# Kernel optimization log

Hardware: AMD Instinct MI355X
Metric: run time of the kernel (lower is better)

The kernel has to match this reference:

```python
import jax, jax.numpy as jnp
import numpy as np

N_NODES = 100000


def _sage_conv(x, src, dst, Wl, Wr, b):
    # mean aggregation of source features onto destination nodes (PyG SAGEConv default)
    msgs = x[src]                                             # [E, d] irregular gather
    agg = jax.ops.segment_sum(msgs, dst, num_segments=N_NODES)
    cnt = jax.ops.segment_sum(jnp.ones((src.shape[0], 1), x.dtype), dst,
                              num_segments=N_NODES)
    agg = agg / jnp.maximum(cnt, 1.0)                         # mean; isolated nodes -> 0
    return agg @ Wl.T + x @ Wr.T + b                          # W_l * agg + W_r * x + b


def setup_inputs() -> dict:
    key = jax.random.key(0)
    ks = jax.random.split(key, 7)
    d_in, d_hid, d_out = 64, 64, 40
    n_edges = 1200000
    x = jax.random.normal(ks[0], (N_NODES, d_in), dtype=jnp.float32)
    edge_index = jax.random.randint(ks[1], (2, n_edges), 0, N_NODES, dtype=jnp.int64)
    s1 = 1.0 / np.sqrt(d_in)
    s2 = 1.0 / np.sqrt(d_hid)
    return {
        "x": x,
        "edge_index": edge_index,
        "W1l": jax.random.normal(ks[2], (d_hid, d_in), dtype=jnp.float32) * s1,
        "W1r": jax.random.normal(ks[3], (d_hid, d_in), dtype=jnp.float32) * s1,
        "b1": jnp.zeros((d_hid,), dtype=jnp.float32),
        "W2l": jax.random.normal(ks[4], (d_out, d_hid), dtype=jnp.float32) * s2,
        "W2r": jax.random.normal(ks[5], (d_out, d_hid), dtype=jnp.float32) * s2,
        "b2": jnp.zeros((d_out,), dtype=jnp.float32),
    }


def reference(x, edge_index, W1l, W1r, b1, W2l, W2r, b2):
    src, dst = edge_index[0], edge_index[1]
    h = _sage_conv(x, src, dst, W1l, W1r, b1)
    h = jax.nn.relu(h)
    # F.dropout(p=0.5) in eval mode is identity (deterministic reference)
    out = _sage_conv(h, src, dst, W2l, W2r, b2)
    return out
```

## Files before the change

kernel.cpp:

```cpp
#include <hip/hip_runtime.h>
#include <hip/hip_bf16.h>

__device__ __forceinline__ float bf2f(unsigned short u) {
    return __uint_as_float(((unsigned int)u) << 16);
}
__device__ __forceinline__ unsigned short f2bf(float f) {
    unsigned int u = __float_as_uint(f);
    return (unsigned short)((u + 0x7FFFu + ((u >> 16) & 1u)) >> 16);
}

__device__ __forceinline__ bool is_i64(const int* __restrict__ e) {
    int z = 0;
#pragma unroll
    for (int i = 0; i < 16; ++i) z |= e[2 * i + 1];
    return z == 0;
}

__global__ void hist_rank_kernel(const int* __restrict__ eidx, int n_edges,
                                 int* __restrict__ deg, int* __restrict__ rank) {
    const int half = (n_edges + 1) / 2;
    const int e = blockIdx.x * blockDim.x + threadIdx.x;
    if (e >= half) return;
    const bool i64 = is_i64(eidx);
    {
        int d = i64 ? eidx[2 * (n_edges + e)] : eidx[n_edges + e];
        rank[e] = atomicAdd(&deg[d], 1);
    }
    const int e2 = e + half;
    if (e2 < n_edges) {
        int d = i64 ? eidx[2 * (n_edges + e2)] : eidx[n_edges + e2];
        rank[e2] = atomicAdd(&deg[d], 1);
    }
}

__global__ void fill_rank_kernel(const int* __restrict__ eidx, int n_edges,
                                 const int* __restrict__ off, const int* __restrict__ rank,
                                 int* __restrict__ csr) {
    const int half = (n_edges + 1) / 2;
    const int e = blockIdx.x * blockDim.x + threadIdx.x;
    if (e >= half) return;
    const bool i64 = is_i64(eidx);
    {
        int s, d;
        if (i64) { s = eidx[2 * e]; d = eidx[2 * (n_edges + e)]; }
        else     { s = eidx[e];     d = eidx[n_edges + e]; }
        __builtin_nontemporal_store(s, &csr[off[d] + rank[e]]);
    }
    const int e2 = e + half;
    if (e2 < n_edges) {
        int s, d;
        if (i64) { s = eidx[2 * e2]; d = eidx[2 * (n_edges + e2)]; }
        else     { s = eidx[e2];     d = eidx[n_edges + e2]; }
        __builtin_nontemporal_store(s, &csr[off[d] + rank[e2]]);
    }
}

__global__ void fill_kernel(const int* __restrict__ eidx, int n_edges,
                            int* __restrict__ cursor, int* __restrict__ csr) {
    int e = blockIdx.x * blockDim.x + threadIdx.x;
    if (e >= n_edges) return;
    const bool i64 = is_i64(eidx);
    int s, d;
    if (i64) { s = eidx[2 * e]; d = eidx[2 * (n_edges + e)]; }
    else     { s = eidx[e];     d = eidx[n_edges + e]; }
    int pos = atomicAdd(&cursor[d], 1);
    csr[pos] = s;
}

#define TILE 1024
__global__ void scan_p1(const int* __restrict__ deg, int* __restrict__ bsum, int n) {
    __shared__ int red[256];
    const int t = threadIdx.x;
    const int base = blockIdx.x * TILE + t * 4;
    int s = 0;
#pragma unroll
    for (int k = 0; k < 4; ++k) { int i = base + k; if (i < n) s += deg[i]; }
    red[t] = s;
    __syncthreads();
    for (int d = 128; d > 0; d >>= 1) {
        if (t < d) red[t] += red[t + d];
        __syncthreads();
    }
    if (t == 0) bsum[blockIdx.x] = red[0];
}

__global__ void scan_p2(int* __restrict__ bsum, int* __restrict__ off, int nb, int n) {
    __shared__ int s[1024];
    const int t = threadIdx.x;
    s[t] = (t < nb) ? bsum[t] : 0;
    __syncthreads();
    for (int d = 1; d < 1024; d <<= 1) {
        int v = (t >= d) ? s[t - d] : 0;
        __syncthreads();
        s[t] += v;
        __syncthreads();
    }
    if (t < nb) bsum[t] = (t == 0) ? 0 : s[t - 1];
    if (t == 0) off[n] = s[nb - 1];
}

__global__ void scan_p3(const int* __restrict__ deg, const int* __restrict__ bsum,
                        int* __restrict__ off, int* __restrict__ cursor, int n) {
    __shared__ int red[256];
    const int t = threadIdx.x;
    const int base = blockIdx.x * TILE + t * 4;
    int v0 = 0, v1 = 0, v2 = 0, v3 = 0;
    if (base + 0 < n) v0 = deg[base + 0];
    if (base + 1 < n) v1 = deg[base + 1];
    if (base + 2 < n) v2 = deg[base + 2];
    if (base + 3 < n) v3 = deg[base + 3];
    const int mysum = v0 + v1 + v2 + v3;
    red[t] = mysum;
    __syncthreads();
    for (int d = 1; d < 256; d <<= 1) {
        int u = (t >= d) ? red[t - d] : 0;
        __syncthreads();
        red[t] += u;
        __syncthreads();
    }
    int run = bsum[blockIdx.x] + red[t] - mysum;
    if (base + 0 < n) { off[base + 0] = run; cursor[base + 0] = run; run += v0; }
    if (base + 1 < n) { off[base + 1] = run; cursor[base + 1] = run; run += v1; }
    if (base + 2 < n) { off[base + 2] = run; cursor[base + 2] = run; run += v2; }
    if (base + 3 < n) { off[base + 3] = run; cursor[base + 3] = run; run += v3; }
}

template <int OUT_DIM, int GST>
__global__ __launch_bounds__(256) void dual_gemm3(
        const float* __restrict__ in,
        const float* __restrict__ Wl, const float* __restrict__ Wr,
        const float* __restrict__ bias,
        unsigned short* __restrict__ gout,
        float* __restrict__ sout,
        int n_nodes) {
    __shared__ unsigned int sWp[64][65];
    __shared__ float sB[OUT_DIM];
    __shared__ float sX[4][8][68];

    for (int idx = threadIdx.x; idx < OUT_DIM * 64; idx += 256) {
        const int r = idx >> 6, c = idx & 63;
        sWp[c][r] = (unsigned int)f2bf(Wl[idx]) | ((unsigned int)f2bf(Wr[idx]) << 16);
    }
    if (threadIdx.x < OUT_DIM) sB[threadIdx.x] = bias[threadIdx.x];
    __syncthreads();

    const int g = threadIdx.x >> 6;
    const int j = threadIdx.x & 63;
    const bool jv = (j < OUT_DIM);
    const int jj = jv ? j : 0;
    const int blockBase = blockIdx.x * 128;

#pragma unroll 1
    for (int it = 0; it < 4; ++it) {
        const int nb = blockBase + it * 32 + g * 8;
        if (nb >= n_nodes) break;
#pragma unroll
        for (int n = 0; n < 8; ++n) {
            const int node = nb + n;
            sX[g][n][j] = (node < n_nodes) ? in[(size_t)node * 64 + j] : 0.0f;
        }
        float al[8], ar[8];
#pragma unroll
        for (int n = 0; n < 8; ++n) { al[n] = 0.0f; ar[n] = 0.0f; }

#pragma unroll 2
        for (int q = 0; q < 16; ++q) {
            const unsigned int w0 = sWp[4 * q + 0][jj];
            const unsigned int w1 = sWp[4 * q + 1][jj];
            const unsigned int w2 = sWp[4 * q + 2][jj];
            const unsigned int w3 = sWp[4 * q + 3][jj];
            const float4 x0 = *(const float4*)&sX[g][0][4 * q];
            const float4 x1 = *(const float4*)&sX[g][1][4 * q];
            const float4 x2 = *(const float4*)&sX[g][2][4 * q];
            const float4 x3 = *(const float4*)&sX[g][3][4 * q];
            const float4 x4 = *(const float4*)&sX[g][4][4 * q];
            const float4 x5 = *(const float4*)&sX[g][5][4 * q];
            const float4 x6 = *(const float4*)&sX[g][6][4 * q];
            const float4 x7 = *(const float4*)&sX[g][7][4 * q];
#define DG_STEP(WP, M)                                                         \
            {                                                                  \
                const float wl_ = __uint_as_float((WP) << 16);                 \
                const float wr_ = __uint_as_float((WP) & 0xFFFF0000u);         \
                al[0] = fmaf(x0.M, wl_, al[0]); ar[0] = fmaf(x0.M, wr_, ar[0]);\
                al[1] = fmaf(x1.M, wl_, al[1]); ar[1] = fmaf(x1.M, wr_, ar[1]);\
                al[2] = fmaf(x2.M, wl_, al[2]); ar[2] = fmaf(x2.M, wr_, ar[2]);\
                al[3] = fmaf(x3.M, wl_, al[3]); ar[3] = fmaf(x3.M, wr_, ar[3]);\
                al[4] = fmaf(x4.M, wl_, al[4]); ar[4] = fmaf(x4.M, wr_, ar[4]);\
                al[5] = fmaf(x5.M, wl_, al[5]); ar[5] = fmaf(x5.M, wr_, ar[5]);\
                al[6] = fmaf(x6.M, wl_, al[6]); ar[6] = fmaf(x6.M, wr_, ar[6]);\
                al[7] = fmaf(x7.M, wl_, al[7]); ar[7] = fmaf(x7.M, wr_, ar[7]);\
            }
            DG_STEP(w0, x)
            DG_STEP(w1, y)
            DG_STEP(w2, z)
            DG_STEP(w3, w)
#undef DG_STEP
        }

        const float bb = jv ? sB[jj] : 0.0f;
#pragma unroll
        for (int n = 0; n < 8; ++n) {
            const int node = nb + n;
            if (node < n_nodes) {
                if (jv) {
                    gout[(size_t)node * GST + j] = f2bf(al[n]);
                    sout[(size_t)node * OUT_DIM + j] = ar[n] + bb;
                } else if (j < GST) {
                    gout[(size_t)node * GST + j] = 0;
                }
            }
        }
    }
}

template <int SRC_STRIDE, int CGROUPS, int OUT_DIM, bool RELU>
__global__ __launch_bounds__(256) void gather_addmul_bf16(
        const unsigned short* __restrict__ gsrc,
        const float* __restrict__ sadd,
        const int* __restrict__ off, const int* __restrict__ csr,
        float* __restrict__ out, int n_nodes) {
    const int l = threadIdx.x & 63;
    const int wave = (int)((blockIdx.x * blockDim.x + threadIdx.x) >> 6);
    const int c = l & 15, r = l >> 4;
    const bool cact = (c < CGROUPS);
    const int n0 = wave * 8;

    for (int n = n0; n < n0 + 8; ++n) {
        if (n >= n_nodes) return;
        const int e0 = off[n], e1 = off[n + 1];
        float4 a0 = {0.f,0.f,0.f,0.f}, a1 = a0, a2 = a0, a3 = a0;
        for (int i = e0; i < e1; i += 16) {
            const int i0 = i + r, i1 = i0 + 4, i2 = i0 + 8, i3 = i0 + 12;
            if (cact && i0 < e1) {
                const int s = csr[i0];
                const ushort4 u = *(const ushort4*)(gsrc + (size_t)s * SRC_STRIDE + 4 * c);
                a0.x += bf2f(u.x); a0.y += bf2f(u.y); a0.z += bf2f(u.z); a0.w += bf2f(u.w);
            }
            if (cact && i1 < e1) {
                const int s = csr[i1];
                const ushort4 u = *(const ushort4*)(gsrc + (size_t)s * SRC_STRIDE + 4 * c);
                a1.x += bf2f(u.x); a1.y += bf2f(u.y); a1.z += bf2f(u.z); a1.w += bf2f(u.w);
            }
            if (cact && i2 < e1) {
                const int s = csr[i2];
                const ushort4 u = *(const ushort4*)(gsrc + (size_t)s * SRC_STRIDE + 4 * c);
                a2.x += bf2f(u.x); a2.y += bf2f(u.y); a2.z += bf2f(u.z); a2.w += bf2f(u.w);
            }
            if (cact && i3 < e1) {
                const int s = csr[i3];
                const ushort4 u = *(const ushort4*)(gsrc + (size_t)s * SRC_STRIDE + 4 * c);
                a3.x += bf2f(u.x); a3.y += bf2f(u.y); a3.z += bf2f(u.z); a3.w += bf2f(u.w);
            }
        }
        float4 a;
        a.x = (a0.x + a1.x) + (a2.x + a3.x);
        a.y = (a0.y + a1.y) + (a2.y + a3.y);
        a.z = (a0.z + a1.z) + (a2.z + a3.z);
        a.w = (a0.w + a1.w) + (a2.w + a3.w);
        a.x += __shfl_xor(a.x, 16); a.y += __shfl_xor(a.y, 16);
        a.z += __shfl_xor(a.z, 16); a.w += __shfl_xor(a.w, 16);
        a.x += __shfl_xor(a.x, 32); a.y += __shfl_xor(a.y, 32);
        a.z += __shfl_xor(a.z, 32); a.w += __shfl_xor(a.w, 32);
        const int deg = e1 - e0;
        const float inv = (deg > 0) ? 1.0f / (float)deg : 0.0f;
        if (4 * l < OUT_DIM) {
            const float4 sv = *(const float4*)(sadd + (size_t)n * OUT_DIM + 4 * l);
            float4 o;
            o.x = fmaf(a.x, inv, sv.x);
            o.y = fmaf(a.y, inv, sv.y);
            o.z = fmaf(a.z, inv, sv.z);
            o.w = fmaf(a.w, inv, sv.w);
            if (RELU) {
                o.x = fmaxf(o.x, 0.f); o.y = fmaxf(o.y, 0.f);
                o.z = fmaxf(o.z, 0.f); o.w = fmaxf(o.w, 0.f);
            }
            *(float4*)(out + (size_t)n * OUT_DIM + 4 * l) = o;
        }
    }
}

#define NPB 32
template <int OUT_DIM, bool RELU>
__global__ __launch_bounds__(512, 8) void fused_layer_f4(
        const float* __restrict__ feat,
        const int* __restrict__ off, const int* __restrict__ csr,
        const float* __restrict__ Wl, const float* __restrict__ Wr,
        const float* __restrict__ bias,
        float* __restrict__ out, int n_nodes) {
    __shared__ float sWl[OUT_DIM][65];
    __shared__ float sWr[OUT_DIM][65];
    __shared__ float sB[OUT_DIM];
    __shared__ float sA[8][64];
    __shared__ float sX[8][64];

    for (int idx = threadIdx.x; idx < OUT_DIM * 64; idx += 512) {
        sWl[idx >> 6][idx & 63] = Wl[idx];
        sWr[idx >> 6][idx & 63] = Wr[idx];
    }
    if (threadIdx.x < OUT_DIM) sB[threadIdx.x] = bias[threadIdx.x];
    __syncthreads();

    const int g = threadIdx.x >> 6;
    const int l = threadIdx.x & 63;
    const int c = l & 15, r = l >> 4;
    const int base = blockIdx.x * NPB;

#pragma unroll 1
    for (int it = 0; it < NPB / 8; ++it) {
        const int node = base + it * 8 + g;
        if (node >= n_nodes) break;
        const int e0 = off[node], e1 = off[node + 1];
        const float selfv = feat[(size_t)node * 64 + l];
        float4 a0 = {0.f,0.f,0.f,0.f}, a1 = a0, a2 = a0, a3 = a0;
        for (int i = e0; i < e1; i += 16) {
            const int i0 = i + r, i1 = i0 + 4, i2 = i0 + 8, i3 = i0 + 12;
            if (i0 < e1) { const int s = csr[i0];
                const float4 v = *(const float4*)(feat + (size_t)s * 64 + 4 * c);
                a0.x += v.x; a0.y += v.y; a0.z += v.z; a0.w += v.w; }
            if (i1 < e1) { const int s = csr[i1];
                const float4 v = *(const float4*)(feat + (size_t)s * 64 + 4 * c);
                a1.x += v.x; a1.y += v.y; a1.z += v.z; a1.w += v.w; }
            if (i2 < e1) { const int s = csr[i2];
                const float4 v = *(const float4*)(feat + (size_t)s * 64 + 4 * c);
                a2.x += v.x; a2.y += v.y; a2.z += v.z; a2.w += v.w; }
            if (i3 < e1) { const int s = csr[i3];
                const float4 v = *(const float4*)(feat + (size_t)s * 64 + 4 * c);
                a3.x += v.x; a3.y += v.y; a3.z += v.z; a3.w += v.w; }
        }
        float4 a;
        a.x = (a0.x + a1.x) + (a2.x + a3.x);
        a.y = (a0.y + a1.y) + (a2.y + a3.y);
        a.z = (a0.z + a1.z) + (a2.z + a3.z);
        a.w = (a0.w + a1.w) + (a2.w + a3.w);
        a.x += __shfl_xor(a.x, 16); a.y += __shfl_xor(a.y, 16);
        a.z += __shfl_xor(a.z, 16); a.w += __shfl_xor(a.w, 16);
        a.x += __shfl_xor(a.x, 32); a.y += __shfl_xor(a.y, 32);
        a.z += __shfl_xor(a.z, 32); a.w += __shfl_xor(a.w, 32);
        const int deg = e1 - e0;
        const float inv = (deg > 0) ? 1.0f / (float)deg : 0.0f;
        if (l < 16) {
            float4 s4;
            s4.x = a.x * inv; s4.y = a.y * inv; s4.z = a.z * inv; s4.w = a.w * inv;
            *(float4*)&sA[g][4 * l] = s4;
        }
        sX[g][l] = selfv;
        if (l < OUT_DIM) {
            float acc = sB[l];
#pragma unroll
            for (int k = 0; k < 64; ++k) {
                acc = fmaf(sA[g][k], sWl[l][k], acc);
                acc = fmaf(sX[g][k], sWr[l][k], acc);
            }
            if (RELU) acc = fmaxf(acc, 0.0f);
            out[(size_t)node * OUT_DIM + l] = acc;
        }
    }
}

template <int OUT_DIM, bool RELU, bool FEAT_BF16, bool OUT_BF16>
__global__ __launch_bounds__(512, 8) void fused_layer(
        const void* __restrict__ feat,
        const int* __restrict__ off, const int* __restrict__ csr,
        const float* __restrict__ Wl, const float* __restrict__ Wr,
        const float* __restrict__ bias,
        void* __restrict__ out, int n_nodes) {
    __shared__ float sWl[OUT_DIM][65];
    __shared__ float sWr[OUT_DIM][65];
    __shared__ float sB[OUT_DIM];
    __shared__ float sA[8][64];
    __shared__ float sX[8][64];

    for (int idx = threadIdx.x; idx < OUT_DIM * 64; idx += 512) {
        sWl[idx >> 6][idx & 63] = Wl[idx];
        sWr[idx >> 6][idx & 63] = Wr[idx];
    }
    if (threadIdx.x < OUT_DIM) sB[threadIdx.x] = bias[threadIdx.x];
    __syncthreads();

    const int g = threadIdx.x >> 6;
    const int j = threadIdx.x & 63;
    const int base = blockIdx.x * NPB;

#pragma unroll 1
    for (int it = 0; it < NPB / 8; ++it) {
        const int node = base + it * 8 + g;
        if (node >= n_nodes) break;
        const int e0 = off[node], e1 = off[node + 1];
        float a0 = 0.f, a1 = 0.f, a2 = 0.f, a3 = 0.f;
        int i = e0;
        while (i < e1) {
            const int cnt = ((e1 - i) < 64) ? (e1 - i) : 64;
            const int eid = (j < cnt) ? csr[i + j] : 0;
            int t = 0;
            for (; t + 3 < cnt; t += 4) {
                const int s0 = __shfl(eid, t);
                const int s1 = __shfl(eid, t + 1);
                const int s2 = __shfl(eid, t + 2);
                const int s3 = __shfl(eid, t + 3);
                if (FEAT_BF16) {
                    a0 += bf2f(((const unsigned short*)feat)[(size_t)s0 * 64 + j]);
                    a1 += bf2f(((const unsigned short*)feat)[(size_t)s1 * 64 + j]);
                    a2 += bf2f(((const unsigned short*)feat)[(size_t)s2 * 64 + j]);
                    a3 += bf2f(((const unsigned short*)feat)[(size_t)s3 * 64 + j]);
                } else {
                    a0 += ((const float*)feat)[(size_t)s0 * 64 + j];
                    a1 += ((const float*)feat)[(size_t)s1 * 64 + j];
                    a2 += ((const float*)feat)[(size_t)s2 * 64 + j];
                    a3 += ((const float*)feat)[(size_t)s3 * 64 + j];
                }
            }
            for (; t < cnt; ++t) {
                const int s0 = __shfl(eid, t);
                a0 += FEAT_BF16 ? bf2f(((const unsigned short*)feat)[(size_t)s0 * 64 + j])
                                : ((const float*)feat)[(size_t)s0 * 64 + j];
            }
            i += cnt;
        }
        const int deg = e1 - e0;
        const float inv = (deg > 0) ? 1.0f / (float)deg : 0.0f;
        sA[g][j] = ((a0 + a1) + (a2 + a3)) * inv;
        sX[g][j] = FEAT_BF16 ? bf2f(((const unsigned short*)feat)[(size_t)node * 64 + j])
                             : ((const float*)feat)[(size_t)node * 64 + j];
        if (j < OUT_DIM) {
            float acc = sB[j];
#pragma unroll
            for (int k = 0; k < 64; ++k) {
                acc = fmaf(sA[g][k], sWl[j][k], acc);
                acc = fmaf(sX[g][k], sWr[j][k], acc);
            }
            if (RELU) acc = fmaxf(acc, 0.0f);
            if (OUT_BF16)
                ((unsigned short*)out)[(size_t)node * OUT_DIM + j] = f2bf(acc);
            else
                ((float*)out)[(size_t)node * OUT_DIM + j] = acc;
        }
    }
}

extern "C" void kernel_launch(void* const* d_in, const int* in_sizes, int n_in,
                              void* d_out, int out_size, void* d_ws, size_t ws_size,
                              hipStream_t stream) {
    const float* x   = (const float*)d_in[0];
    const int*   ei  = (const int*)d_in[1];
    const float* W1l = (const float*)d_in[2];
    const float* W1r = (const float*)d_in[3];
    const float* b1  = (const float*)d_in[4];
    const float* W2l = (const float*)d_in[5];
    const float* W2r = (const float*)d_in[6];
    const float* b2  = (const float*)d_in[7];
    float* out = (float*)d_out;

    const int n_nodes = in_sizes[0] / 64;
    const int n_edges = in_sizes[1] / 2;

    const size_t off_b  = (size_t)(n_nodes + 1) * sizeof(int);
    const size_t cur_b  = (size_t)n_nodes * sizeof(int);
    const size_t csr_b  = (size_t)n_edges * sizeof(int);
    const size_t rank_b = (size_t)n_edges * sizeof(int);
    const size_t bsum_b = 1024 * sizeof(int);
    const size_t g1_b   = (size_t)n_nodes * 64 * sizeof(unsigned short);
    const size_t s1_b   = (size_t)n_nodes * 64 * sizeof(float);
    const size_t g2_b   = (size_t)n_nodes * 48 * sizeof(unsigned short);
    const size_t h_b    = (size_t)n_nodes * 64 * sizeof(float);
    const size_t reg1_b = g1_b + s1_b;

    char* p = (char*)d_ws;
    int* off    = (int*)p;  p += off_b;
    int* cursor = (int*)p;  p += cur_b;
    int* csr    = (int*)p;  p += csr_b;
    int* rank   = (int*)p;  p += rank_b;
    int* bsum   = (int*)p;  p += bsum_b;
    size_t used = ((size_t)(p - (char*)d_ws) + 255) / 256 * 256;
    p = (char*)d_ws + used;

    const bool tierA = ws_size >= used + reg1_b + h_b;
    const bool tierC = ws_size >= used + h_b;

    unsigned short* g1 = (unsigned short*)p;
    float*          s1 = (float*)(p + g1_b);
    float*          h  = (float*)(p + reg1_b);
    unsigned short* g2 = (unsigned short*)p;
    float*          s2 = (float*)(p + g2_b);

    hipMemsetAsync(cursor, 0, cur_b, stream);
    const int half = (n_edges + 1) / 2;
    const int hblocks = (half + 255) / 256;
    hist_rank_kernel<<<hblocks, 256, 0, stream>>>(ei, n_edges, cursor, rank);
    const int nb = (n_nodes + TILE - 1) / TILE;
    scan_p1<<<nb, 256, 0, stream>>>(cursor, bsum, n_nodes);
    scan_p2<<<1, 1024, 0, stream>>>(bsum, off, nb, n_nodes);
    scan_p3<<<nb, 256, 0, stream>>>(cursor, bsum, off, cursor, n_nodes);

    const int eblocks = (n_edges + 255) / 256;
    if (tierA) {
        fill_rank_kernel<<<hblocks, 256, 0, stream>>>(ei, n_edges, off, rank, csr);
    } else {
        fill_kernel<<<eblocks, 256, 0, stream>>>(ei, n_edges, cursor, csr);
    }

    const int gemmBlocks   = (n_nodes + 127) / 128;
    const int gatherBlocks = (n_nodes + 31) / 32;
    const int fusedBlocks  = (n_nodes + NPB - 1) / NPB;

    if (tierA) {
        dual_gemm3<64, 64><<<gemmBlocks, 256, 0, stream>>>(
            x, W1l, W1r, b1, g1, s1, n_nodes);
        gather_addmul_bf16<64, 16, 64, true><<<gatherBlocks, 256, 0, stream>>>(
            g1, s1, off, csr, h, n_nodes);
        dual_gemm3<40, 48><<<gemmBlocks, 256, 0, stream>>>(
            h, W2l, W2r, b2, g2, s2, n_nodes);
        gather_addmul_bf16<48, 10, 40, false><<<gatherBlocks, 256, 0, stream>>>(
            g2, s2, off, csr, out, n_nodes);
    } else if (tierC) {
        float* hh = (float*)p;
        fused_layer_f4<64, true><<<fusedBlocks, 512, 0, stream>>>(
            x, off, csr, W1l, W1r, b1, hh, n_nodes);
        fused_layer_f4<40, false><<<fusedBlocks, 512, 0, stream>>>(
            hh, off, csr, W2l, W2r, b2, out, n_nodes);
    } else {
        void* hh = (void*)p;
        fused_layer<64, true, false, true><<<fusedBlocks, 512, 0, stream>>>(
            x, off, csr, W1l, W1r, b1, hh, n_nodes);
        fused_layer<40, false, true, false><<<fusedBlocks, 512, 0, stream>>>(
            hh, off, csr, W2l, W2r, b2, out, n_nodes);
    }
}
```

Measured before the change: 317.5 us.

## Fuse layer-1 dual GEMM with degree histogram into one launch

```diff
diff --git a/kernel.cpp b/kernel.cpp
--- a/kernel.cpp
+++ b/kernel.cpp
@@ -14,6 +14,111 @@
 #pragma unroll
     for (int i = 0; i < 16; ++i) z |= e[2 * i + 1];
     return z == 0;
+}
+
+template <int OUT_DIM, int GST>
+__global__ __launch_bounds__(256) void gemm1_hist_fused(
+        const float* __restrict__ in, const float* __restrict__ Wl,
+        const float* __restrict__ Wr, const float* __restrict__ bias,
+        unsigned short* __restrict__ gout, float* __restrict__ sout,
+        int n_nodes, int gemmBlocks,
+        const int* __restrict__ eidx, int n_edges,
+        int* __restrict__ deg, int* __restrict__ rank) {
+    __shared__ unsigned int sWp[64][65];
+    __shared__ float sB[OUT_DIM];
+    __shared__ float sX[4][8][68];
+
+    if ((int)blockIdx.x >= gemmBlocks) {
+        const int half = (n_edges + 1) / 2;
+        const int e = (blockIdx.x - gemmBlocks) * blockDim.x + threadIdx.x;
+        if (e >= half) return;
+        const bool i64 = is_i64(eidx);
+        {
+            int d = i64 ? eidx[2 * (n_edges + e)] : eidx[n_edges + e];
+            rank[e] = atomicAdd(&deg[d], 1);
+        }
+        const int e2 = e + half;
+        if (e2 < n_edges) {
+            int d = i64 ? eidx[2 * (n_edges + e2)] : eidx[n_edges + e2];
+            rank[e2] = atomicAdd(&deg[d], 1);
+        }
+        return;
+    }
+
+    for (int idx = threadIdx.x; idx < OUT_DIM * 64; idx += 256) {
+        const int r = idx >> 6, c = idx & 63;
+        sWp[c][r] = (unsigned int)f2bf(Wl[idx]) | ((unsigned int)f2bf(Wr[idx]) << 16);
+    }
+    if (threadIdx.x < OUT_DIM) sB[threadIdx.x] = bias[threadIdx.x];
+    __syncthreads();
+
+    const int g = threadIdx.x >> 6;
+    const int j = threadIdx.x & 63;
+    const bool jv = (j < OUT_DIM);
+    const int jj = jv ? j : 0;
+    const int blockBase = blockIdx.x * 128;
+
+#pragma unroll 1
+    for (int it = 0; it < 4; ++it) {
+        const int nb = blockBase + it * 32 + g * 8;
+        if (nb >= n_nodes) break;
+#pragma unroll
+        for (int n = 0; n < 8; ++n) {
+            const int node = nb + n;
+            sX[g][n][j] = (node < n_nodes) ? in[(size_t)node * 64 + j] : 0.0f;
+        }
+        float al[8], ar[8];
+#pragma unroll
+        for (int n = 0; n < 8; ++n) { al[n] = 0.0f; ar[n] = 0.0f; }
+
+#pragma unroll 2
+        for (int q = 0; q < 16; ++q) {
+            const unsigned int w0 = sWp[4 * q + 0][jj];
+            const unsigned int w1 = sWp[4 * q + 1][jj];
+            const unsigned int w2 = sWp[4 * q + 2][jj];
+            const unsigned int w3 = sWp[4 * q + 3][jj];
+            const float4 x0 = *(const float4*)&sX[g][0][4 * q];
+            const float4 x1 = *(const float4*)&sX[g][1][4 * q];
+            const float4 x2 = *(const float4*)&sX[g][2][4 * q];
+            const float4 x3 = *(const float4*)&sX[g][3][4 * q];
+            const float4 x4 = *(const float4*)&sX[g][4][4 * q];
+            const float4 x5 = *(const float4*)&sX[g][5][4 * q];
+            const float4 x6 = *(const float4*)&sX[g][6][4 * q];
+            const float4 x7 = *(const float4*)&sX[g][7][4 * q];
+#define DG_STEP(WP, M)                                                         \
+            {                                                                  \
+                const float wl_ = __uint_as_float((WP) << 16);                 \
+                const float wr_ = __uint_as_float((WP) & 0xFFFF0000u);         \
+                al[0] = fmaf(x0.M, wl_, al[0]); ar[0] = fmaf(x0.M, wr_, ar[0]);\
+                al[1] = fmaf(x1.M, wl_, al[1]); ar[1] = fmaf(x1.M, wr_, ar[1]);\
+                al[2] = fmaf(x2.M, wl_, al[2]); ar[2] = fmaf(x2.M, wr_, ar[2]);\
+                al[3] = fmaf(x3.M, wl_, al[3]); ar[3] = fmaf(x3.M, wr_, ar[3]);\
+                al[4] = fmaf(x4.M, wl_, al[4]); ar[4] = fmaf(x4.M, wr_, ar[4]);\
+                al[5] = fmaf(x5.M, wl_, al[5]); ar[5] = fmaf(x5.M, wr_, ar[5]);\
+                al[6] = fmaf(x6.M, wl_, al[6]); ar[6] = fmaf(x6.M, wr_, ar[6]);\
+                al[7] = fmaf(x7.M, wl_, al[7]); ar[7] = fmaf(x7.M, wr_, ar[7]);\
+            }
+            DG_STEP(w0, x)
+            DG_STEP(w1, y)
+            DG_STEP(w2, z)
+            DG_STEP(w3, w)
+#undef DG_STEP
+        }
+
+        const float bb = jv ? sB[jj] : 0.0f;
+#pragma unroll
+        for (int n = 0; n < 8; ++n) {
+            const int node = nb + n;
+            if (node < n_nodes) {
+                if (jv) {
+                    gout[(size_t)node * GST + j] = f2bf(al[n]);
+                    sout[(size_t)node * OUT_DIM + j] = ar[n] + bb;
+                } else if (j < GST) {
+                    gout[(size_t)node * GST + j] = 0;
+                }
+            }
+        }
+    }
 }
 
 __global__ void hist_rank_kernel(const int* __restrict__ eidx, int n_edges,
@@ -483,45 +588,49 @@
     float*          s2 = (float*)(p + g2_b);
 
     hipMemsetAsync(cursor, 0, cur_b, stream);
+
     const int half = (n_edges + 1) / 2;
     const int hblocks = (half + 255) / 256;
-    hist_rank_kernel<<<hblocks, 256, 0, stream>>>(ei, n_edges, cursor, rank);
-    const int nb = (n_nodes + TILE - 1) / TILE;
-    scan_p1<<<nb, 256, 0, stream>>>(cursor, bsum, n_nodes);
-    scan_p2<<<1, 1024, 0, stream>>>(bsum, off, nb, n_nodes);
-    scan_p3<<<nb, 256, 0, stream>>>(cursor, bsum, off, cursor, n_nodes);
-
-    const int eblocks = (n_edges + 255) / 256;
-    if (tierA) {
-        fill_rank_kernel<<<hblocks, 256, 0, stream>>>(ei, n_edges, off, rank, csr);
-    } else {
-        fill_kernel<<<eblocks, 256, 0, stream>>>(ei, n_edges, cursor, csr);
-    }
-
     const int gemmBlocks   = (n_nodes + 127) / 128;
     const int gatherBlocks = (n_nodes + 31) / 32;
     const int fusedBlocks  = (n_nodes + NPB - 1) / NPB;
+    const int nb = (n_nodes + TILE - 1) / TILE;
+    const int eblocks = (n_edges + 255) / 256;
 
     if (tierA) {
-        dual_gemm3<64, 64><<<gemmBlocks, 256, 0, stream>>>(
-            x, W1l, W1r, b1, g1, s1, n_nodes);
+        gemm1_hist_fused<64, 64><<<gemmBlocks + hblocks, 256, 0, stream>>>(
+            x, W1l, W1r, b1, g1, s1, n_nodes, gemmBlocks,
+            ei, n_edges, cursor, rank);
+        scan_p1<<<nb, 256, 0, stream>>>(cursor, bsum, n_nodes);
+        scan_p2<<<1, 1024, 0, stream>>>(bsum, off, nb, n_nodes);
+        scan_p3<<<nb, 256, 0, stream>>>(cursor, bsum, off, cursor, n_nodes);
+        fill_rank_kernel<<<hblocks, 256, 0, stream>>>(ei, n_edges, off, rank, csr);
+
         gather_addmul_bf16<64, 16, 64, true><<<gatherBlocks, 256, 0, stream>>>(
             g1, s1, off, csr, h, n_nodes);
         dual_gemm3<40, 48><<<gemmBlocks, 256, 0, stream>>>(
             h, W2l, W2r, b2, g2, s2, n_nodes);
         gather_addmul_bf16<48, 10, 40, false><<<gatherBlocks, 256, 0, stream>>>(
             g2, s2, off, csr, out, n_nodes);
-    } else if (tierC) {
-        float* hh = (float*)p;
-        fused_layer_f4<64, true><<<fusedBlocks, 512, 0, stream>>>(
-            x, off, csr, W1l, W1r, b1, hh, n_nodes);
-        fused_layer_f4<40, false><<<fusedBlocks, 512, 0, stream>>>(
-            hh, off, csr, W2l, W2r, b2, out, n_nodes);
     } else {
-        void* hh = (void*)p;
-        fused_layer<64, true, false, true><<<fusedBlocks, 512, 0, stream>>>(
-            x, off, csr, W1l, W1r, b1, hh, n_nodes);
-        fused_layer<40, false, true, false><<<fusedBlocks, 512, 0, stream>>>(
-            hh, off, csr, W2l, W2r, b2, out, n_nodes);
-    }
-}
+        hist_rank_kernel<<<hblocks, 256, 0, stream>>>(ei, n_edges, cursor, rank);
+        scan_p1<<<nb, 256, 0, stream>>>(cursor, bsum, n_nodes);
+        scan_p2<<<1, 1024, 0, stream>>>(bsum, off, nb, n_nodes);
+        scan_p3<<<nb, 256, 0, stream>>>(cursor, bsum, off, cursor, n_nodes);
+        fill_kernel<<<eblocks, 256, 0, stream>>>(ei, n_edges, cursor, csr);
+
+        if (tierC) {
+            float* hh = (float*)p;
+            fused_layer_f4<64, true><<<fusedBlocks, 512, 0, stream>>>(
+                x, off, csr, W1l, W1r, b1, hh, n_nodes);
+            fused_layer_f4<40, false><<<fusedBlocks, 512, 0, stream>>>(
+                hh, off, csr, W2l, W2r, b2, out, n_nodes);
+        } else {
+            void* hh = (void*)p;
+            fused_layer<64, true, false, true><<<fusedBlocks, 512, 0, stream>>>(
+                x, off, csr, W1l, W1r, b1, hh, n_nodes);
+            fused_layer<40, false, true, false><<<fusedBlocks, 512, 0, stream>>>(
+                hh, off, csr, W2l, W2r, b2, out, n_nodes);
+        }
+    }
+}
```

After: 285.3 us. 1.11x faster.
